# Optimization experiments

Hardware: AMD Instinct MI355X
Metric: run time of the kernel (lower is better)

## Reference

```python
import jax, jax.numpy as jnp
import numpy as np

B = 2048          # puzzles
E_PER = 1620      # 81 cells * 20 constraint neighbors
N = B * 81        # total nodes
NFEAT = 10


def _winit(key, fan_in, fan_out):
    s = (1.0 / np.sqrt(fan_in)).astype(np.float32) if isinstance(fan_in, np.ndarray) else 1.0 / np.sqrt(fan_in)
    return jax.random.uniform(key, (fan_in, fan_out), jnp.float32, -s, s)


def setup_inputs() -> dict:
    key = jax.random.key(0)
    ks = jax.random.split(key, 20)
    x = jax.random.normal(ks[0], (N, NFEAT), jnp.float32)
    # batched edge index [B, 2, E_PER]; values are global node ids
    edge_index = jax.random.randint(ks[1], (B, 2, E_PER), 0, N, dtype=jnp.int32)
    dims = [(NFEAT, 16), (16, 32), (32, 64), (64, 32), (32, 16)]
    params = {}
    for i, (ci, co) in enumerate(dims, start=1):
        params[f'W{i}'] = _winit(ks[2 * i], ci, co)
        params[f'b{i}'] = jnp.zeros((co,), jnp.float32)
    params['fW1'] = _winit(ks[14], 16, 16)
    params['fb1'] = jnp.zeros((16,), jnp.float32)
    params['fW2'] = _winit(ks[15], 16, 9)
    params['fb2'] = jnp.zeros((9,), jnp.float32)
    return {'x': x, 'edge_index': edge_index, **params}


def _gcn(h, W, b, src, dst, norm):
    # GCNConv: out[i] = sum_{j->i} norm_ij * (h_j W) + b   (self-loops included in src/dst)
    h = h @ W                                  # [N, Cout] small GEMM
    msg = h[src] * norm[:, None]               # gather + scale, [E+N, Cout]
    return jax.ops.segment_sum(msg, dst, num_segments=N) + b


def reference(x, edge_index, W1, b1, W2, b2, W3, b3, W4, b4, W5, b5, fW1, fb1, fW2, fb2):
    # replicate edge_index.permute(1,2,0).reshape(2,-1)
    ei = jnp.transpose(edge_index, (1, 2, 0)).reshape(2, -1)
    src, dst = ei[0], ei[1]
    # add self loops (PyG gcn_norm default)
    loop = jnp.arange(N, dtype=src.dtype)
    src = jnp.concatenate([src, loop])
    dst = jnp.concatenate([dst, loop])
    deg = jax.ops.segment_sum(jnp.ones(src.shape, x.dtype), dst, num_segments=N)
    dinv = jnp.where(deg > 0, jax.lax.rsqrt(jnp.maximum(deg, 1e-12)), 0.0)
    norm = dinv[src] * dinv[dst]               # shared across layers (same graph)
    h = jax.nn.relu(_gcn(x, W1, b1, src, dst, norm))
    h = jax.nn.relu(_gcn(h, W2, b2, src, dst, norm))
    h = jax.nn.relu(_gcn(h, W3, b3, src, dst, norm))
    h = jax.nn.relu(_gcn(h, W4, b4, src, dst, norm))
    h = jax.nn.relu(_gcn(h, W5, b5, src, dst, norm))
    h = h.reshape(-1, 16)
    h = jax.nn.relu(h @ fW1 + fb1)
    h = h @ fW2 + fb2
    return h.reshape(-1, 81, 9)
```

## Files before the change

### kernel.cpp

```cpp
#include <hip/hip_runtime.h>
#include <hip/hip_fp16.h>


#define NN    165888
#define NBAT  2048
#define EPER  1620
#define NEDGE (NBAT * EPER)
#define ETOT  (NEDGE + NN)
#define NBKT  648
#define NBLK  512
#define SCATE (4 * EPER)
#define SLICE 20736
#define BCAP  6144


__device__ inline void blk_scan256(int val, int& excl, int& total, int* sw) {
  int lane = threadIdx.x & 63, w = threadIdx.x >> 6;
  int x = val;
#pragma unroll
  for (int off = 1; off < 64; off <<= 1) {
    int y = __shfl_up(x, off);
    if (lane >= off) x += y;
  }
  if (lane == 63) sw[w] = x;
  __syncthreads();
  int woff = 0;
  if (w > 0) woff = sw[0];
  if (w > 1) woff += sw[1];
  if (w > 2) woff += sw[2];
  total = sw[0] + sw[1] + sw[2] + sw[3];
  excl = woff + x - val;
}

__device__ inline void pbase_scan(const int* __restrict__ btot, int* pb, int* sw) {
  int t = threadIdx.x;
  int e0 = 0, e1 = 0, e2 = 0, s = 0;
  if (t < 216) {
    e0 = btot[3 * t]; e1 = btot[3 * t + 1]; e2 = btot[3 * t + 2];
    s = e0 + e1 + e2;
  }
  int excl, tot;
  blk_scan256(s, excl, tot, sw);
  if (t < 216) {
    pb[3 * t]     = excl;
    pb[3 * t + 1] = excl + e0;
    pb[3 * t + 2] = excl + e0 + e1;
  }
  __syncthreads();
}


__global__ __launch_bounds__(256) void k_count(const int* __restrict__ ei,
                                               int* __restrict__ counts) {
  __shared__ int cnt[NBKT];
  int t = threadIdx.x;
  for (int k = t; k < NBKT; k += 256) cnt[k] = 0;
  __syncthreads();
  int b0 = blockIdx.x * 4;
  for (int b = b0; b < b0 + 4; ++b) {
    const int* dstp = ei + (size_t)b * (2 * EPER) + EPER;
    for (int e = t; e < EPER; e += 256) atomicAdd(&cnt[dstp[e] >> 8], 1);
  }
  __syncthreads();
  for (int k = t; k < NBKT; k += 256) counts[blockIdx.x * NBKT + k] = cnt[k];
}

__global__ __launch_bounds__(256) void k_scan(const int* __restrict__ counts,
                                              int* __restrict__ basesT,
                                              int* __restrict__ btot) {
  int bkt = blockIdx.x, t = threadIdx.x;
  int a = counts[(2 * t)     * NBKT + bkt];
  int b = counts[(2 * t + 1) * NBKT + bkt];
  __shared__ int sw[4];
  int excl, tot;
  blk_scan256(a + b, excl, tot, sw);
  basesT[bkt * NBLK + 2 * t]     = excl;
  basesT[bkt * NBLK + 2 * t + 1] = excl + a;
  if (t == 255) btot[bkt] = tot;
}

__global__ __launch_bounds__(256) void k_scat(const int* __restrict__ ei,
                                              const int* __restrict__ basesT,
                                              const int* __restrict__ btot,
                                              unsigned int* __restrict__ pairs) {
  __shared__ int pb[NBKT];
  __shared__ int sw[4];
  __shared__ int cnt[NBKT];
  __shared__ int lcur[NBKT];
  __shared__ int gdst[NBKT];
  __shared__ unsigned int sorted[SCATE];
  __shared__ unsigned short sbkt[SCATE];
  int t = threadIdx.x;
  for (int k = t; k < NBKT; k += 256) cnt[k] = 0;
  pbase_scan(btot, pb, sw);
  int b0 = blockIdx.x * 4;
  for (int b = b0; b < b0 + 4; ++b) {
    const int* dstp = ei + (size_t)b * (2 * EPER) + EPER;
    for (int e = t; e < EPER; e += 256) atomicAdd(&cnt[dstp[e] >> 8], 1);
  }
  __syncthreads();
  {
    int e0 = 0, e1 = 0, e2 = 0, s = 0;
    if (t < 216) {
      e0 = cnt[3 * t]; e1 = cnt[3 * t + 1]; e2 = cnt[3 * t + 2];
      s = e0 + e1 + e2;
    }
    int excl, tot;
    blk_scan256(s, excl, tot, sw);
    if (t < 216) {
      cnt[3 * t]     = excl;
      cnt[3 * t + 1] = excl + e0;
      cnt[3 * t + 2] = excl + e0 + e1;
    }
  }
  __syncthreads();
  for (int k = t; k < NBKT; k += 256) {
    int loc = cnt[k];
    gdst[k] = pb[k] + basesT[k * NBLK + blockIdx.x] - loc;
    lcur[k] = loc;
  }
  __syncthreads();
  for (int b = b0; b < b0 + 4; ++b) {
    const int* srcp = ei + (size_t)b * (2 * EPER);
    const int* dstp = srcp + EPER;
    for (int e = t; e < EPER; e += 256) {
      int d = dstp[e];
      int bk = d >> 8;
      int pos = atomicAdd(&lcur[bk], 1);
      sorted[pos] = (unsigned int)srcp[e] | ((unsigned int)(d & 255) << 24);
      sbkt[pos]   = (unsigned short)bk;
    }
  }
  __syncthreads();
  for (int k = t; k < SCATE; k += 256)
    pairs[gdst[sbkt[k]] + k] = sorted[k];
}

__global__ __launch_bounds__(256) void k_build(const unsigned int* __restrict__ pairs,
                                               const int* __restrict__ btot,
                                               const float* __restrict__ x,
                                               const float* __restrict__ W1,
                                               int* __restrict__ row_start,
                                               int* __restrict__ row_end,
                                               float* __restrict__ dinv,
                                               int* __restrict__ csr,
                                               __half* __restrict__ g0) {
  __shared__ int pb[NBKT];
  __shared__ int sw[4];
  __shared__ int cnt[256];
  __shared__ unsigned int sp[BCAP];
  __shared__ float sW[160];
  int bkt = blockIdx.x, t = threadIdx.x;
  cnt[t] = 0;
  if (t < 160) sW[t] = W1[t];
  pbase_scan(btot, pb, sw);
  int p0 = pb[bkt];
  int n  = btot[bkt];
  for (int k = t; k < n; k += 256) {
    unsigned int pr = pairs[p0 + k];
    if (k < BCAP) sp[k] = pr;
    atomicAdd(&cnt[pr >> 24], 1);
  }
  __syncthreads();
  int indeg = cnt[t];
  int excl, tot;
  blk_scan256(indeg, excl, tot, sw);
  int csrbase = p0 + bkt * 256;
  int rs   = csrbase + excl + t;
  int node = bkt * 256 + t;
  int d    = indeg + 1;
  float di = rsqrtf((float)d);
  row_start[node] = rs;
  row_end[node]   = rs + d;
  dinv[node] = di;
  csr[rs] = node;
  __syncthreads();
  cnt[t] = rs + 1;
  __syncthreads();
  for (int k = t; k < n; k += 256) {
    unsigned int pr = (k < BCAP) ? sp[k] : pairs[p0 + k];
    int pos = atomicAdd(&cnt[pr >> 24], 1);
    csr[pos] = (int)(pr & 0x00FFFFFFu);
  }
  float r[10];
#pragma unroll
  for (int k = 0; k < 10; ++k) r[k] = x[(size_t)node * 10 + k];
  float acc[16];
#pragma unroll
  for (int j = 0; j < 16; ++j) acc[j] = 0.0f;
#pragma unroll
  for (int k = 0; k < 10; ++k) {
    float rv = r[k];
#pragma unroll
    for (int j = 0; j < 16; ++j) acc[j] = fmaf(rv, sW[k * 16 + j], acc[j]);
  }
  __half* op = g0 + (size_t)node * 16;
  union { int4 v; __half2 h[4]; } pk;
#pragma unroll
  for (int half8 = 0; half8 < 2; ++half8) {
#pragma unroll
    for (int j = 0; j < 4; ++j)
      pk.h[j] = __floats2half2_rn(acc[half8 * 8 + 2 * j] * di,
                                  acc[half8 * 8 + 2 * j + 1] * di);
    *(int4*)(op + half8 * 8) = pk.v;
  }
}


template <int C, int EPI>
__device__ inline float4 agg_core_h(const __half* __restrict__ g,
                                    const int* __restrict__ csr,
                                    int rs, int re, int q, int gl) {
  constexpr int LG = C / 4;
  float4 acc = make_float4(0.f, 0.f, 0.f, 0.f);
  const __half* gq = g + (size_t)q * 4;
  int iters = 0;
  for (int p = rs; p < re; p += EPI) {
    ++iters;
    int m[EPI / LG];
#pragma unroll
    for (int u = 0; u < EPI / LG; ++u) {
      int idx = p + u * LG + q;
      m[u] = csr[idx < re ? idx : re - 1];
    }
    float2 v[EPI];
#pragma unroll
    for (int j = 0; j < EPI; ++j) {
      int s = __shfl(m[j / LG], gl + (j % LG));
      v[j] = *(const float2*)(gq + (size_t)s * C);
    }
#pragma unroll
    for (int j = 0; j < EPI; ++j) {
      const __half2* hp = (const __half2*)&v[j];
      float2 lo = __half22float2(hp[0]);
      float2 hi = __half22float2(hp[1]);
      acc.x += lo.x; acc.y += lo.y; acc.z += hi.x; acc.w += hi.y;
    }
  }
  float dups = (float)(iters * EPI - (re - rs));
  int slast = csr[re - 1];
  float2 vl = *(const float2*)(gq + (size_t)slast * C);
  const __half2* hp = (const __half2*)&vl;
  float2 lo = __half22float2(hp[0]);
  float2 hi = __half22float2(hp[1]);
  acc.x = fmaf(-dups, lo.x, acc.x);
  acc.y = fmaf(-dups, lo.y, acc.y);
  acc.z = fmaf(-dups, hi.x, acc.z);
  acc.w = fmaf(-dups, hi.y, acc.w);
  return acc;
}


__global__ __launch_bounds__(256) void k_agg_ep16(const __half* __restrict__ g,
                                                  const int* __restrict__ row_start,
                                                  const int* __restrict__ row_end,
                                                  const int* __restrict__ csr,
                                                  const float* __restrict__ dinv,
                                                  const float* __restrict__ bias,
                                                  __half* __restrict__ out) {
  constexpr int LG = 4, NPB = 64, SPB = SLICE / NPB;
  int t  = threadIdx.x;
  int q  = t & (LG - 1);
  int bi = blockIdx.x;
  int vb = (bi & 7) * SPB + (bi >> 3);
  int i  = vb * NPB + t / LG;
  int gl = (t & 63) & ~(LG - 1);
  float4 acc = agg_core_h<16, 16>(g, csr, row_start[i], row_end[i], q, gl);
  float di = dinv[i];
  float4 bb = *(const float4*)(bias + q * 4);
  acc.x = fmaxf(fmaf(di, acc.x, bb.x), 0.f) * di;
  acc.y = fmaxf(fmaf(di, acc.y, bb.y), 0.f) * di;
  acc.z = fmaxf(fmaf(di, acc.z, bb.z), 0.f) * di;
  acc.w = fmaxf(fmaf(di, acc.w, bb.w), 0.f) * di;
  union { int2 v; __half2 h[2]; } pk;
  pk.h[0] = __floats2half2_rn(acc.x, acc.y);
  pk.h[1] = __floats2half2_rn(acc.z, acc.w);
  *(int2*)(out + (size_t)i * 16 + q * 4) = pk.v;
}


__global__ __launch_bounds__(256) void k_agg_g2(const __half* __restrict__ g,
                                                const int* __restrict__ row_start,
                                                const int* __restrict__ row_end,
                                                const int* __restrict__ csr,
                                                const float* __restrict__ dinv,
                                                const float* __restrict__ W2,
                                                const float* __restrict__ b2,
                                                __half* __restrict__ out) {
  constexpr int CI = 16, CO = 32, LG = 4, NPB = 64, SPB = SLICE / NPB, RP = 20;
  __shared__ float sW[CI * CO];
  __shared__ float sB[CO];
  __shared__ float rows[NPB * RP];
  __shared__ float sdi[NPB];
  int t = threadIdx.x;
  for (int k = t; k < CI * CO; k += 256) sW[k] = W2[k];
  if (t < CO) sB[t] = b2[t];
  int bi = blockIdx.x;
  int vb = (bi & 7) * SPB + (bi >> 3);
  int nbase = vb * NPB;
  int q = t & (LG - 1), nl = t / LG;
  int i = nbase + nl;
  int gl = (t & 63) & ~(LG - 1);
  float4 acc = agg_core_h<16, 16>(g, csr, row_start[i], row_end[i], q, gl);
  float di = dinv[i];
  acc.x *= di; acc.y *= di; acc.z *= di; acc.w *= di;
  *(float4*)&rows[nl * RP + q * 4] = acc;
  if (q == 0) sdi[nl] = di;
  __syncthreads();
  int n2 = t >> 2, c = t & 3;
  float o[8];
#pragma unroll
  for (int j = 0; j < 8; ++j) o[j] = sB[c * 8 + j];
  const float* row = &rows[n2 * RP];
#pragma unroll
  for (int k = 0; k < CI; ++k) {
    float rv = row[k];
#pragma unroll
    for (int j = 0; j < 8; ++j) o[j] = fmaf(rv, sW[k * CO + c * 8 + j], o[j]);
  }
  float d2 = sdi[n2];
#pragma unroll
  for (int j = 0; j < 8; ++j) o[j] = fmaxf(o[j], 0.f) * d2;
  union { int4 v; __half2 h[4]; } pk;
#pragma unroll
  for (int j = 0; j < 4; ++j) pk.h[j] = __floats2half2_rn(o[2 * j], o[2 * j + 1]);
  *(int4*)(out + (size_t)(nbase + n2) * 32 + c * 8) = pk.v;
}


__global__ __launch_bounds__(256) void k_agg_g34(const __half* __restrict__ g,
                                                 const int* __restrict__ row_start,
                                                 const int* __restrict__ row_end,
                                                 const int* __restrict__ csr,
                                                 const float* __restrict__ dinv,
                                                 const float* __restrict__ W3,
                                                 const float* __restrict__ b3,
                                                 const float* __restrict__ W4,
                                                 __half* __restrict__ out) {
  constexpr int LG = 8, NPB = 32, SPB = SLICE / NPB, RP = 36, HP = 68;
  __shared__ float sW3[32 * 64];
  __shared__ float sW4[64 * 32];
  __shared__ float sB3[64];
  __shared__ float rows[NPB * RP];
  __shared__ float hrows[NPB * HP];
  __shared__ float sdi[NPB];
  int t = threadIdx.x;
  for (int k = t; k < 2048; k += 256) { sW3[k] = W3[k]; sW4[k] = W4[k]; }
  if (t < 64) sB3[t] = b3[t];
  int bi = blockIdx.x;
  int vb = (bi & 7) * SPB + (bi >> 3);
  int nbase = vb * NPB;
  int q = t & (LG - 1), nl = t / LG;
  int i = nbase + nl;
  int gl = (t & 63) & ~(LG - 1);
  float4 acc = agg_core_h<32, 16>(g, csr, row_start[i], row_end[i], q, gl);
  float di = dinv[i];
  acc.x *= di; acc.y *= di; acc.z *= di; acc.w *= di;
  *(float4*)&rows[nl * RP + q * 4] = acc;
  if (q == 0) sdi[nl] = di;
  __syncthreads();
  int n2 = t >> 3, c = t & 7;
  {
    float o[8];
#pragma unroll
    for (int j = 0; j < 8; ++j) o[j] = sB3[c * 8 + j];
    const float* row = &rows[n2 * RP];
#pragma unroll
    for (int k = 0; k < 32; ++k) {
      float rv = row[k];
#pragma unroll
      for (int j = 0; j < 8; ++j) o[j] = fmaf(rv, sW3[k * 64 + c * 8 + j], o[j]);
    }
    float* hp = &hrows[n2 * HP + c * 8];
#pragma unroll
    for (int j = 0; j < 8; ++j) hp[j] = fmaxf(o[j], 0.f);
  }
  __syncthreads();
  {
    float o[4] = {0.f, 0.f, 0.f, 0.f};
    const float* hp = &hrows[n2 * HP];
#pragma unroll
    for (int k = 0; k < 64; ++k) {
      float hv = hp[k];
#pragma unroll
      for (int j = 0; j < 4; ++j) o[j] = fmaf(hv, sW4[k * 32 + c * 4 + j], o[j]);
    }
    float d2 = sdi[n2];
#pragma unroll
    for (int j = 0; j < 4; ++j) o[j] *= d2;
    union { int2 v; __half2 h[2]; } pk;
    pk.h[0] = __floats2half2_rn(o[0], o[1]);
    pk.h[1] = __floats2half2_rn(o[2], o[3]);
    *(int2*)(out + (size_t)(nbase + n2) * 32 + c * 4) = pk.v;
  }
}


__global__ __launch_bounds__(256) void k_agg_g5(const __half* __restrict__ g,
                                                const int* __restrict__ row_start,
                                                const int* __restrict__ row_end,
                                                const int* __restrict__ csr,
                                                const float* __restrict__ dinv,
                                                const float* __restrict__ b4,
                                                const float* __restrict__ W5,
                                                __half* __restrict__ out) {
  constexpr int LG = 8, NPB = 32, SPB = SLICE / NPB, RP = 36;
  __shared__ float sW[32 * 16];
  __shared__ float rows[NPB * RP];
  __shared__ float sdi[NPB];
  int t = threadIdx.x;
  for (int k = t; k < 512; k += 256) sW[k] = W5[k];
  int bi = blockIdx.x;
  int vb = (bi & 7) * SPB + (bi >> 3);
  int nbase = vb * NPB;
  int q = t & (LG - 1), nl = t / LG;
  int i = nbase + nl;
  int gl = (t & 63) & ~(LG - 1);
  float4 acc = agg_core_h<32, 16>(g, csr, row_start[i], row_end[i], q, gl);
  float di = dinv[i];
  float4 bb = *(const float4*)(b4 + q * 4);
  acc.x = fmaxf(fmaf(di, acc.x, bb.x), 0.f);
  acc.y = fmaxf(fmaf(di, acc.y, bb.y), 0.f);
  acc.z = fmaxf(fmaf(di, acc.z, bb.z), 0.f);
  acc.w = fmaxf(fmaf(di, acc.w, bb.w), 0.f);
  *(float4*)&rows[nl * RP + q * 4] = acc;
  if (q == 0) sdi[nl] = di;
  __syncthreads();
  int n2 = t >> 3, c = t & 7;
  float o0 = 0.f, o1 = 0.f;
  const float* row = &rows[n2 * RP];
#pragma unroll
  for (int k = 0; k < 32; ++k) {
    float rv = row[k];
    o0 = fmaf(rv, sW[k * 16 + c * 2],     o0);
    o1 = fmaf(rv, sW[k * 16 + c * 2 + 1], o1);
  }
  float d2 = sdi[n2];
  *(__half2*)(out + (size_t)(nbase + n2) * 16 + c * 2)
      = __floats2half2_rn(o0 * d2, o1 * d2);
}


__global__ __launch_bounds__(256) void k_agg_mlp(const __half* __restrict__ g,
                                                 const int* __restrict__ row_start,
                                                 const int* __restrict__ row_end,
                                                 const int* __restrict__ csr,
                                                 const float* __restrict__ dinv,
                                                 const float* __restrict__ b5,
                                                 const float* __restrict__ fW1,
                                                 const float* __restrict__ fb1,
                                                 const float* __restrict__ fW2,
                                                 const float* __restrict__ fb2,
                                                 float* __restrict__ out) {
  constexpr int LG = 4, NPB = 64, SPB = SLICE / NPB, RP = 20;
  __shared__ float sW1[256], sW2[144], sB1[16], sB2[9];
  __shared__ float rows[NPB * RP];
  __shared__ float zrows[NPB * RP];
  __shared__ float ost[NPB * 9];
  int t = threadIdx.x;
  sW1[t] = fW1[t];
  if (t < 144) sW2[t] = fW2[t];
  if (t < 16)  sB1[t] = fb1[t];
  if (t < 9)   sB2[t] = fb2[t];
  int bi = blockIdx.x;
  int vb = (bi & 7) * SPB + (bi >> 3);
  int nbase = vb * NPB;
  int q = t & (LG - 1), nl = t / LG;
  int i = nbase + nl;
  int gl = (t & 63) & ~(LG - 1);
  float4 acc = agg_core_h<16, 16>(g, csr, row_start[i], row_end[i], q, gl);
  float di = dinv[i];
  float4 bb = *(const float4*)(b5 + q * 4);
  acc.x = fmaxf(fmaf(di, acc.x, bb.x), 0.f);
  acc.y = fmaxf(fmaf(di, acc.y, bb.y), 0.f);
  acc.z = fmaxf(fmaf(di, acc.z, bb.z), 0.f);
  acc.w = fmaxf(fmaf(di, acc.w, bb.w), 0.f);
  *(float4*)&rows[nl * RP + q * 4] = acc;
  __syncthreads();
  int n2 = t >> 2, c = t & 3;
  {
    float o[4];
#pragma unroll
    for (int j = 0; j < 4; ++j) o[j] = sB1[c * 4 + j];
    const float* row = &rows[n2 * RP];
#pragma unroll
    for (int k = 0; k < 16; ++k) {
      float rv = row[k];
#pragma unroll
      for (int j = 0; j < 4; ++j) o[j] = fmaf(rv, sW1[k * 16 + c * 4 + j], o[j]);
    }
    float* zp = &zrows[n2 * RP + c * 4];
#pragma unroll
    for (int j = 0; j < 4; ++j) zp[j] = fmaxf(o[j], 0.f);
  }
  __syncthreads();
  if (c < 3) {
    float o[3];
#pragma unroll
    for (int j = 0; j < 3; ++j) o[j] = sB2[c * 3 + j];
    const float* zp = &zrows[n2 * RP];
#pragma unroll
    for (int k = 0; k < 16; ++k) {
      float zv = zp[k];
#pragma unroll
      for (int j = 0; j < 3; ++j) o[j] = fmaf(zv, sW2[k * 9 + c * 3 + j], o[j]);
    }
#pragma unroll
    for (int j = 0; j < 3; ++j) ost[n2 * 9 + c * 3 + j] = o[j];
  }
  __syncthreads();
  float* ob = out + (size_t)nbase * 9;
  for (int k = t; k < NPB * 9; k += 256) ob[k] = ost[k];
}


extern "C" void kernel_launch(void* const* d_in, const int* in_sizes, int n_in,
                              void* d_out, int out_size, void* d_ws, size_t ws_size,
                              hipStream_t stream) {
  const float* x   = (const float*)d_in[0];
  const int*   ei  = (const int*)d_in[1];
  const float* W1  = (const float*)d_in[2];
  const float* b1  = (const float*)d_in[3];
  const float* W2  = (const float*)d_in[4];
  const float* b2  = (const float*)d_in[5];
  const float* W3  = (const float*)d_in[6];
  const float* b3  = (const float*)d_in[7];
  const float* W4  = (const float*)d_in[8];
  const float* b4  = (const float*)d_in[9];
  const float* W5  = (const float*)d_in[10];
  const float* b5  = (const float*)d_in[11];
  const float* fW1 = (const float*)d_in[12];
  const float* fb1 = (const float*)d_in[13];
  const float* fW2 = (const float*)d_in[14];
  const float* fb2 = (const float*)d_in[15];
  float* out = (float*)d_out;

  char* ws = (char*)d_ws;
  size_t off = 0;
  auto alloc = [&](size_t bytes) -> char* {
    char* p = ws + off;
    off += (bytes + 255) & ~(size_t)255;
    return p;
  };
  int*   counts  = (int*)  alloc((size_t)NBLK * NBKT * 4);
  int*   basesT  = (int*)  alloc((size_t)NBKT * NBLK * 4);
  int*   btot    = (int*)  alloc((size_t)NBKT * 4);
  unsigned int* pairs = (unsigned int*)alloc((size_t)NEDGE * 4);
  int*   rs_     = (int*)  alloc((size_t)NN * 4);
  int*   re_     = (int*)  alloc((size_t)NN * 4);
  float* dinv    = (float*)alloc((size_t)NN * 4);
  int*   csr     = (int*)  alloc((size_t)ETOT * 4);
  __half* H16a   = (__half*)alloc((size_t)NN * 16 * 2);
  __half* H16b   = (__half*)alloc((size_t)NN * 16 * 2);
  __half* H32a   = (__half*)alloc((size_t)NN * 32 * 2);
  __half* H32b   = (__half*)alloc((size_t)NN * 32 * 2);

  k_count<<<NBLK, 256, 0, stream>>>(ei, counts);
  k_scan <<<NBKT, 256, 0, stream>>>(counts, basesT, btot);
  k_scat <<<NBLK, 256, 0, stream>>>(ei, basesT, btot, pairs);
  k_build<<<NBKT, 256, 0, stream>>>(pairs, btot, x, W1, rs_, re_, dinv, csr, H16a);

  k_agg_ep16<<<NN / 64, 256, 0, stream>>>(H16a, rs_, re_, csr, dinv, b1, H16b);
  k_agg_g2<<<NN / 64, 256, 0, stream>>>(H16b, rs_, re_, csr, dinv, W2, b2, H32a);
  k_agg_g34<<<NN / 32, 256, 0, stream>>>(H32a, rs_, re_, csr, dinv, W3, b3, W4, H32b);
  k_agg_g5<<<NN / 32, 256, 0, stream>>>(H32b, rs_, re_, csr, dinv, b4, W5, H16a);
  k_agg_mlp<<<NN / 64, 256, 0, stream>>>(H16a, rs_, re_, csr, dinv, b5,
                                         fW1, fb1, fW2, fb2, out);
}
```

Measured before the change: 365.8 us.

## Widen per-lane gathers to 8 halfs and double nodes per block in aggregation kernels

The aggregation core now has each lane load 16 bytes (8 half channels) per neighbor instead of 8 bytes, so each node uses half as many lanes and each block covers twice as many nodes. Grid sizes are halved, edges per iteration drop from 16 to 8, and the fused dense epilogues are remapped so each thread computes twice as many outputs. The shared-memory row padding changes to odd strides (17/33/65) to avoid bank conflicts. The aim is fewer, wider memory transactions and less shuffle and index overhead per edge, at the cost of higher register pressure and less parallelism per node.

```diff
diff --git a/kernel.cpp b/kernel.cpp
--- a/kernel.cpp
+++ b/kernel.cpp
@@ -208,12 +208,14 @@
 
 
 template <int C, int EPI>
-__device__ inline float4 agg_core_h(const __half* __restrict__ g,
+__device__ inline void agg_core_h16(const __half* __restrict__ g,
                                     const int* __restrict__ csr,
-                                    int rs, int re, int q, int gl) {
-  constexpr int LG = C / 4;
-  float4 acc = make_float4(0.f, 0.f, 0.f, 0.f);
-  const __half* gq = g + (size_t)q * 4;
+                                    int rs, int re, int q, int gl,
+                                    float4& outLo, float4& outHi) {
+  constexpr int LG = C / 8;
+  float4 aLo = make_float4(0.f, 0.f, 0.f, 0.f);
+  float4 aHi = make_float4(0.f, 0.f, 0.f, 0.f);
+  const __half* gq = g + (size_t)q * 8;
   int iters = 0;
   for (int p = rs; p < re; p += EPI) {
     ++iters;
@@ -223,31 +225,36 @@
       int idx = p + u * LG + q;
       m[u] = csr[idx < re ? idx : re - 1];
     }
-    float2 v[EPI];
+    float4 v[EPI];
 #pragma unroll
     for (int j = 0; j < EPI; ++j) {
       int s = __shfl(m[j / LG], gl + (j % LG));
-      v[j] = *(const float2*)(gq + (size_t)s * C);
+      v[j] = *(const float4*)(gq + (size_t)s * C);
     }
 #pragma unroll
     for (int j = 0; j < EPI; ++j) {
       const __half2* hp = (const __half2*)&v[j];
-      float2 lo = __half22float2(hp[0]);
-      float2 hi = __half22float2(hp[1]);
-      acc.x += lo.x; acc.y += lo.y; acc.z += hi.x; acc.w += hi.y;
+      float2 f0 = __half22float2(hp[0]);
+      float2 f1 = __half22float2(hp[1]);
+      float2 f2 = __half22float2(hp[2]);
+      float2 f3 = __half22float2(hp[3]);
+      aLo.x += f0.x; aLo.y += f0.y; aLo.z += f1.x; aLo.w += f1.y;
+      aHi.x += f2.x; aHi.y += f2.y; aHi.z += f3.x; aHi.w += f3.y;
     }
   }
   float dups = (float)(iters * EPI - (re - rs));
   int slast = csr[re - 1];
-  float2 vl = *(const float2*)(gq + (size_t)slast * C);
+  float4 vl = *(const float4*)(gq + (size_t)slast * C);
   const __half2* hp = (const __half2*)&vl;
-  float2 lo = __half22float2(hp[0]);
-  float2 hi = __half22float2(hp[1]);
-  acc.x = fmaf(-dups, lo.x, acc.x);
-  acc.y = fmaf(-dups, lo.y, acc.y);
-  acc.z = fmaf(-dups, hi.x, acc.z);
-  acc.w = fmaf(-dups, hi.y, acc.w);
-  return acc;
+  float2 f0 = __half22float2(hp[0]);
+  float2 f1 = __half22float2(hp[1]);
+  float2 f2 = __half22float2(hp[2]);
+  float2 f3 = __half22float2(hp[3]);
+  aLo.x = fmaf(-dups, f0.x, aLo.x); aLo.y = fmaf(-dups, f0.y, aLo.y);
+  aLo.z = fmaf(-dups, f1.x, aLo.z); aLo.w = fmaf(-dups, f1.y, aLo.w);
+  aHi.x = fmaf(-dups, f2.x, aHi.x); aHi.y = fmaf(-dups, f2.y, aHi.y);
+  aHi.z = fmaf(-dups, f3.x, aHi.z); aHi.w = fmaf(-dups, f3.y, aHi.w);
+  outLo = aLo; outHi = aHi;
 }
 
 
@@ -258,24 +265,33 @@
                                                   const float* __restrict__ dinv,
                                                   const float* __restrict__ bias,
                                                   __half* __restrict__ out) {
-  constexpr int LG = 4, NPB = 64, SPB = SLICE / NPB;
+  constexpr int NPB = 128, SPB = SLICE / NPB;
   int t  = threadIdx.x;
-  int q  = t & (LG - 1);
+  int q  = t & 1;
   int bi = blockIdx.x;
   int vb = (bi & 7) * SPB + (bi >> 3);
-  int i  = vb * NPB + t / LG;
-  int gl = (t & 63) & ~(LG - 1);
-  float4 acc = agg_core_h<16, 16>(g, csr, row_start[i], row_end[i], q, gl);
+  int i  = vb * NPB + t / 2;
+  int gl = (t & 63) & ~1;
+  float4 aLo, aHi;
+  agg_core_h16<16, 8>(g, csr, row_start[i], row_end[i], q, gl, aLo, aHi);
   float di = dinv[i];
-  float4 bb = *(const float4*)(bias + q * 4);
-  acc.x = fmaxf(fmaf(di, acc.x, bb.x), 0.f) * di;
-  acc.y = fmaxf(fmaf(di, acc.y, bb.y), 0.f) * di;
-  acc.z = fmaxf(fmaf(di, acc.z, bb.z), 0.f) * di;
-  acc.w = fmaxf(fmaf(di, acc.w, bb.w), 0.f) * di;
-  union { int2 v; __half2 h[2]; } pk;
-  pk.h[0] = __floats2half2_rn(acc.x, acc.y);
-  pk.h[1] = __floats2half2_rn(acc.z, acc.w);
-  *(int2*)(out + (size_t)i * 16 + q * 4) = pk.v;
+  const float* bp = bias + q * 8;
+  float4 b0 = *(const float4*)bp;
+  float4 b1 = *(const float4*)(bp + 4);
+  aLo.x = fmaxf(fmaf(di, aLo.x, b0.x), 0.f) * di;
+  aLo.y = fmaxf(fmaf(di, aLo.y, b0.y), 0.f) * di;
+  aLo.z = fmaxf(fmaf(di, aLo.z, b0.z), 0.f) * di;
+  aLo.w = fmaxf(fmaf(di, aLo.w, b0.w), 0.f) * di;
+  aHi.x = fmaxf(fmaf(di, aHi.x, b1.x), 0.f) * di;
+  aHi.y = fmaxf(fmaf(di, aHi.y, b1.y), 0.f) * di;
+  aHi.z = fmaxf(fmaf(di, aHi.z, b1.z), 0.f) * di;
+  aHi.w = fmaxf(fmaf(di, aHi.w, b1.w), 0.f) * di;
+  union { int4 v; __half2 h[4]; } pk;
+  pk.h[0] = __floats2half2_rn(aLo.x, aLo.y);
+  pk.h[1] = __floats2half2_rn(aLo.z, aLo.w);
+  pk.h[2] = __floats2half2_rn(aHi.x, aHi.y);
+  pk.h[3] = __floats2half2_rn(aHi.z, aHi.w);
+  *(int4*)(out + (size_t)i * 16 + q * 8) = pk.v;
 }
 
 
@@ -287,7 +303,7 @@
                                                 const float* __restrict__ W2,
                                                 const float* __restrict__ b2,
                                                 __half* __restrict__ out) {
-  constexpr int CI = 16, CO = 32, LG = 4, NPB = 64, SPB = SLICE / NPB, RP = 20;
+  constexpr int CI = 16, CO = 32, NPB = 128, SPB = SLICE / NPB, RP = 17;
   __shared__ float sW[CI * CO];
   __shared__ float sB[CO];
   __shared__ float rows[NPB * RP];
@@ -298,33 +314,41 @@
   int bi = blockIdx.x;
   int vb = (bi & 7) * SPB + (bi >> 3);
   int nbase = vb * NPB;
-  int q = t & (LG - 1), nl = t / LG;
+  int q = t & 1, nl = t / 2;
   int i = nbase + nl;
-  int gl = (t & 63) & ~(LG - 1);
-  float4 acc = agg_core_h<16, 16>(g, csr, row_start[i], row_end[i], q, gl);
+  int gl = (t & 63) & ~1;
+  float4 aLo, aHi;
+  agg_core_h16<16, 8>(g, csr, row_start[i], row_end[i], q, gl, aLo, aHi);
   float di = dinv[i];
-  acc.x *= di; acc.y *= di; acc.z *= di; acc.w *= di;
-  *(float4*)&rows[nl * RP + q * 4] = acc;
+  aLo.x *= di; aLo.y *= di; aLo.z *= di; aLo.w *= di;
+  aHi.x *= di; aHi.y *= di; aHi.z *= di; aHi.w *= di;
+  *(float4*)&rows[nl * RP + q * 8]     = aLo;
+  *(float4*)&rows[nl * RP + q * 8 + 4] = aHi;
   if (q == 0) sdi[nl] = di;
   __syncthreads();
-  int n2 = t >> 2, c = t & 3;
-  float o[8];
-#pragma unroll
-  for (int j = 0; j < 8; ++j) o[j] = sB[c * 8 + j];
+  int n2 = t >> 1, c = t & 1;
+  float o[16];
+#pragma unroll
+  for (int j = 0; j < 16; ++j) o[j] = sB[c * 16 + j];
   const float* row = &rows[n2 * RP];
 #pragma unroll
   for (int k = 0; k < CI; ++k) {
     float rv = row[k];
 #pragma unroll
-    for (int j = 0; j < 8; ++j) o[j] = fmaf(rv, sW[k * CO + c * 8 + j], o[j]);
+    for (int j = 0; j < 16; ++j) o[j] = fmaf(rv, sW[k * CO + c * 16 + j], o[j]);
   }
   float d2 = sdi[n2];
 #pragma unroll
-  for (int j = 0; j < 8; ++j) o[j] = fmaxf(o[j], 0.f) * d2;
+  for (int j = 0; j < 16; ++j) o[j] = fmaxf(o[j], 0.f) * d2;
+  __half* op = out + (size_t)(nbase + n2) * 32 + c * 16;
   union { int4 v; __half2 h[4]; } pk;
 #pragma unroll
-  for (int j = 0; j < 4; ++j) pk.h[j] = __floats2half2_rn(o[2 * j], o[2 * j + 1]);
-  *(int4*)(out + (size_t)(nbase + n2) * 32 + c * 8) = pk.v;
+  for (int half8 = 0; half8 < 2; ++half8) {
+#pragma unroll
+    for (int j = 0; j < 4; ++j)
+      pk.h[j] = __floats2half2_rn(o[half8 * 8 + 2 * j], o[half8 * 8 + 2 * j + 1]);
+    *(int4*)(op + half8 * 8) = pk.v;
+  }
 }
 
 
@@ -337,7 +361,7 @@
                                                  const float* __restrict__ b3,
                                                  const float* __restrict__ W4,
                                                  __half* __restrict__ out) {
-  constexpr int LG = 8, NPB = 32, SPB = SLICE / NPB, RP = 36, HP = 68;
+  constexpr int NPB = 64, SPB = SLICE / NPB, RP = 33, HP = 65;
   __shared__ float sW3[32 * 64];
   __shared__ float sW4[64 * 32];
   __shared__ float sB3[64];
@@ -350,48 +374,50 @@
   int bi = blockIdx.x;
   int vb = (bi & 7) * SPB + (bi >> 3);
   int nbase = vb * NPB;
-  int q = t & (LG - 1), nl = t / LG;
+  int q = t & 3, nl = t / 4;
   int i = nbase + nl;
-  int gl = (t & 63) & ~(LG - 1);
-  float4 acc = agg_core_h<32, 16>(g, csr, row_start[i], row_end[i], q, gl);
+  int gl = (t & 63) & ~3;
+  float4 aLo, aHi;
+  agg_core_h16<32, 8>(g, csr, row_start[i], row_end[i], q, gl, aLo, aHi);
   float di = dinv[i];
-  acc.x *= di; acc.y *= di; acc.z *= di; acc.w *= di;
-  *(float4*)&rows[nl * RP + q * 4] = acc;
+  aLo.x *= di; aLo.y *= di; aLo.z *= di; aLo.w *= di;
+  aHi.x *= di; aHi.y *= di; aHi.z *= di; aHi.w *= di;
+  *(float4*)&rows[nl * RP + q * 8]     = aLo;
+  *(float4*)&rows[nl * RP + q * 8 + 4] = aHi;
   if (q == 0) sdi[nl] = di;
   __syncthreads();
-  int n2 = t >> 3, c = t & 7;
+  int n2 = t >> 2, c = t & 3;
   {
-    float o[8];
-#pragma unroll
-    for (int j = 0; j < 8; ++j) o[j] = sB3[c * 8 + j];
+    float o[16];
+#pragma unroll
+    for (int j = 0; j < 16; ++j) o[j] = sB3[c * 16 + j];
     const float* row = &rows[n2 * RP];
 #pragma unroll
     for (int k = 0; k < 32; ++k) {
       float rv = row[k];
 #pragma unroll
-      for (int j = 0; j < 8; ++j) o[j] = fmaf(rv, sW3[k * 64 + c * 8 + j], o[j]);
-    }
-    float* hp = &hrows[n2 * HP + c * 8];
-#pragma unroll
-    for (int j = 0; j < 8; ++j) hp[j] = fmaxf(o[j], 0.f);
+      for (int j = 0; j < 16; ++j) o[j] = fmaf(rv, sW3[k * 64 + c * 16 + j], o[j]);
+    }
+    float* hp = &hrows[n2 * HP + c * 16];
+#pragma unroll
+    for (int j = 0; j < 16; ++j) hp[j] = fmaxf(o[j], 0.f);
   }
   __syncthreads();
   {
-    float o[4] = {0.f, 0.f, 0.f, 0.f};
+    float o[8] = {0.f, 0.f, 0.f, 0.f, 0.f, 0.f, 0.f, 0.f};
     const float* hp = &hrows[n2 * HP];
 #pragma unroll
     for (int k = 0; k < 64; ++k) {
       float hv = hp[k];
 #pragma unroll
-      for (int j = 0; j < 4; ++j) o[j] = fmaf(hv, sW4[k * 32 + c * 4 + j], o[j]);
+      for (int j = 0; j < 8; ++j) o[j] = fmaf(hv, sW4[k * 32 + c * 8 + j], o[j]);
     }
     float d2 = sdi[n2];
-#pragma unroll
-    for (int j = 0; j < 4; ++j) o[j] *= d2;
-    union { int2 v; __half2 h[2]; } pk;
-    pk.h[0] = __floats2half2_rn(o[0], o[1]);
-    pk.h[1] = __floats2half2_rn(o[2], o[3]);
-    *(int2*)(out + (size_t)(nbase + n2) * 32 + c * 4) = pk.v;
+    union { int4 v; __half2 h[4]; } pk;
+#pragma unroll
+    for (int j = 0; j < 4; ++j)
+      pk.h[j] = __floats2half2_rn(o[2 * j] * d2, o[2 * j + 1] * d2);
+    *(int4*)(out + (size_t)(nbase + n2) * 32 + c * 8) = pk.v;
   }
 }
 
@@ -404,7 +430,7 @@
                                                 const float* __restrict__ b4,
                                                 const float* __restrict__ W5,
                                                 __half* __restrict__ out) {
-  constexpr int LG = 8, NPB = 32, SPB = SLICE / NPB, RP = 36;
+  constexpr int NPB = 64, SPB = SLICE / NPB, RP = 33;
   __shared__ float sW[32 * 16];
   __shared__ float rows[NPB * RP];
   __shared__ float sdi[NPB];
@@ -413,31 +439,41 @@
   int bi = blockIdx.x;
   int vb = (bi & 7) * SPB + (bi >> 3);
   int nbase = vb * NPB;
-  int q = t & (LG - 1), nl = t / LG;
+  int q = t & 3, nl = t / 4;
   int i = nbase + nl;
-  int gl = (t & 63) & ~(LG - 1);
-  float4 acc = agg_core_h<32, 16>(g, csr, row_start[i], row_end[i], q, gl);
+  int gl = (t & 63) & ~3;
+  float4 aLo, aHi;
+  agg_core_h16<32, 8>(g, csr, row_start[i], row_end[i], q, gl, aLo, aHi);
   float di = dinv[i];
-  float4 bb = *(const float4*)(b4 + q * 4);
-  acc.x = fmaxf(fmaf(di, acc.x, bb.x), 0.f);
-  acc.y = fmaxf(fmaf(di, acc.y, bb.y), 0.f);
-  acc.z = fmaxf(fmaf(di, acc.z, bb.z), 0.f);
-  acc.w = fmaxf(fmaf(di, acc.w, bb.w), 0.f);
-  *(float4*)&rows[nl * RP + q * 4] = acc;
+  const float* bp = b4 + q * 8;
+  float4 b0 = *(const float4*)bp;
+  float4 b1 = *(const float4*)(bp + 4);
+  aLo.x = fmaxf(fmaf(di, aLo.x, b0.x), 0.f);
+  aLo.y = fmaxf(fmaf(di, aLo.y, b0.y), 0.f);
+  aLo.z = fmaxf(fmaf(di, aLo.z, b0.z), 0.f);
+  aLo.w = fmaxf(fmaf(di, aLo.w, b0.w), 0.f);
+  aHi.x = fmaxf(fmaf(di, aHi.x, b1.x), 0.f);
+  aHi.y = fmaxf(fmaf(di, aHi.y, b1.y), 0.f);
+  aHi.z = fmaxf(fmaf(di, aHi.z, b1.z), 0.f);
+  aHi.w = fmaxf(fmaf(di, aHi.w, b1.w), 0.f);
+  *(float4*)&rows[nl * RP + q * 8]     = aLo;
+  *(float4*)&rows[nl * RP + q * 8 + 4] = aHi;
   if (q == 0) sdi[nl] = di;
   __syncthreads();
-  int n2 = t >> 3, c = t & 7;
-  float o0 = 0.f, o1 = 0.f;
+  int n2 = t >> 2, c = t & 3;
+  float o[4] = {0.f, 0.f, 0.f, 0.f};
   const float* row = &rows[n2 * RP];
 #pragma unroll
   for (int k = 0; k < 32; ++k) {
     float rv = row[k];
-    o0 = fmaf(rv, sW[k * 16 + c * 2],     o0);
-    o1 = fmaf(rv, sW[k * 16 + c * 2 + 1], o1);
+#pragma unroll
+    for (int j = 0; j < 4; ++j) o[j] = fmaf(rv, sW[k * 16 + c * 4 + j], o[j]);
   }
   float d2 = sdi[n2];
-  *(__half2*)(out + (size_t)(nbase + n2) * 16 + c * 2)
-      = __floats2half2_rn(o0 * d2, o1 * d2);
+  union { int2 v; __half2 h[2]; } pk;
+  pk.h[0] = __floats2half2_rn(o[0] * d2, o[1] * d2);
+  pk.h[1] = __floats2half2_rn(o[2] * d2, o[3] * d2);
+  *(int2*)(out + (size_t)(nbase + n2) * 16 + c * 4) = pk.v;
 }
 
 
@@ -452,7 +488,7 @@
                                                  const float* __restrict__ fW2,
                                                  const float* __restrict__ fb2,
                                                  float* __restrict__ out) {
-  constexpr int LG = 4, NPB = 64, SPB = SLICE / NPB, RP = 20;
+  constexpr int NPB = 128, SPB = SLICE / NPB, RP = 17;
   __shared__ float sW1[256], sW2[144], sB1[16], sB2[9];
   __shared__ float rows[NPB * RP];
   __shared__ float zrows[NPB * RP];
@@ -465,48 +501,70 @@
   int bi = blockIdx.x;
   int vb = (bi & 7) * SPB + (bi >> 3);
   int nbase = vb * NPB;
-  int q = t & (LG - 1), nl = t / LG;
+  int q = t & 1, nl = t / 2;
   int i = nbase + nl;
-  int gl = (t & 63) & ~(LG - 1);
-  float4 acc = agg_core_h<16, 16>(g, csr, row_start[i], row_end[i], q, gl);
+  int gl = (t & 63) & ~1;
+  float4 aLo, aHi;
+  agg_core_h16<16, 8>(g, csr, row_start[i], row_end[i], q, gl, aLo, aHi);
   float di = dinv[i];
-  float4 bb = *(const float4*)(b5 + q * 4);
-  acc.x = fmaxf(fmaf(di, acc.x, bb.x), 0.f);
-  acc.y = fmaxf(fmaf(di, acc.y, bb.y), 0.f);
-  acc.z = fmaxf(fmaf(di, acc.z, bb.z), 0.f);
-  acc.w = fmaxf(fmaf(di, acc.w, bb.w), 0.f);
-  *(float4*)&rows[nl * RP + q * 4] = acc;
-  __syncthreads();
-  int n2 = t >> 2, c = t & 3;
+  const float* bp = b5 + q * 8;
+  float4 b0 = *(const float4*)bp;
+  float4 b1 = *(const float4*)(bp + 4);
+  aLo.x = fmaxf(fmaf(di, aLo.x, b0.x), 0.f);
+  aLo.y = fmaxf(fmaf(di, aLo.y, b0.y), 0.f);
+  aLo.z = fmaxf(fmaf(di, aLo.z, b0.z), 0.f);
+  aLo.w = fmaxf(fmaf(di, aLo.w, b0.w), 0.f);
+  aHi.x = fmaxf(fmaf(di, aHi.x, b1.x), 0.f);
+  aHi.y = fmaxf(fmaf(di, aHi.y, b1.y), 0.f);
+  aHi.z = fmaxf(fmaf(di, aHi.z, b1.z), 0.f);
+  aHi.w = fmaxf(fmaf(di, aHi.w, b1.w), 0.f);
+  *(float4*)&rows[nl * RP + q * 8]     = aLo;
+  *(float4*)&rows[nl * RP + q * 8 + 4] = aHi;
+  __syncthreads();
+  int n2 = t >> 1, c = t & 1;
   {
-    float o[4];
-#pragma unroll
-    for (int j = 0; j < 4; ++j) o[j] = sB1[c * 4 + j];
+    float o[8];
+#pragma unroll
+    for (int j = 0; j < 8; ++j) o[j] = sB1[c * 8 + j];
     const float* row = &rows[n2 * RP];
 #pragma unroll
     for (int k = 0; k < 16; ++k) {
       float rv = row[k];
 #pragma unroll
-      for (int j = 0; j < 4; ++j) o[j] = fmaf(rv, sW1[k * 16 + c * 4 + j], o[j]);
-    }
-    float* zp = &zrows[n2 * RP + c * 4];
-#pragma unroll
-    for (int j = 0; j < 4; ++j) zp[j] = fmaxf(o[j], 0.f);
-  }
-  __syncthreads();
-  if (c < 3) {
-    float o[3];
-#pragma unroll
-    for (int j = 0; j < 3; ++j) o[j] = sB2[c * 3 + j];
+      for (int j = 0; j < 8; ++j) o[j] = fmaf(rv, sW1[k * 16 + c * 8 + j], o[j]);
+    }
+    float* zp = &zrows[n2 * RP + c * 8];
+#pragma unroll
+    for (int j = 0; j < 8; ++j) zp[j] = fmaxf(o[j], 0.f);
+  }
+  __syncthreads();
+  {
     const float* zp = &zrows[n2 * RP];
-#pragma unroll
-    for (int k = 0; k < 16; ++k) {
-      float zv = zp[k];
-#pragma unroll
-      for (int j = 0; j < 3; ++j) o[j] = fmaf(zv, sW2[k * 9 + c * 3 + j], o[j]);
-    }
-#pragma unroll
-    for (int j = 0; j < 3; ++j) ost[n2 * 9 + c * 3 + j] = o[j];
+    if (c == 0) {
+      float o[5];
+#pragma unroll
+      for (int j = 0; j < 5; ++j) o[j] = sB2[j];
+#pragma unroll
+      for (int k = 0; k < 16; ++k) {
+        float zv = zp[k];
+#pragma unroll
+        for (int j = 0; j < 5; ++j) o[j] = fmaf(zv, sW2[k * 9 + j], o[j]);
+      }
+#pragma unroll
+      for (int j = 0; j < 5; ++j) ost[n2 * 9 + j] = o[j];
+    } else {
+      float o[4];
+#pragma unroll
+      for (int j = 0; j < 4; ++j) o[j] = sB2[5 + j];
+#pragma unroll
+      for (int k = 0; k < 16; ++k) {
+        float zv = zp[k];
+#pragma unroll
+        for (int j = 0; j < 4; ++j) o[j] = fmaf(zv, sW2[k * 9 + 5 + j], o[j]);
+      }
+#pragma unroll
+      for (int j = 0; j < 4; ++j) ost[n2 * 9 + 5 + j] = o[j];
+    }
   }
   __syncthreads();
   float* ob = out + (size_t)nbase * 9;
@@ -560,10 +618,10 @@
   k_scat <<<NBLK, 256, 0, stream>>>(ei, basesT, btot, pairs);
   k_build<<<NBKT, 256, 0, stream>>>(pairs, btot, x, W1, rs_, re_, dinv, csr, H16a);
 
-  k_agg_ep16<<<NN / 64, 256, 0, stream>>>(H16a, rs_, re_, csr, dinv, b1, H16b);
-  k_agg_g2<<<NN / 64, 256, 0, stream>>>(H16b, rs_, re_, csr, dinv, W2, b2, H32a);
-  k_agg_g34<<<NN / 32, 256, 0, stream>>>(H32a, rs_, re_, csr, dinv, W3, b3, W4, H32b);
-  k_agg_g5<<<NN / 32, 256, 0, stream>>>(H32b, rs_, re_, csr, dinv, b4, W5, H16a);
-  k_agg_mlp<<<NN / 64, 256, 0, stream>>>(H16a, rs_, re_, csr, dinv, b5,
-                                         fW1, fb1, fW2, fb2, out);
-}
+  k_agg_ep16<<<NN / 128, 256, 0, stream>>>(H16a, rs_, re_, csr, dinv, b1, H16b);
+  k_agg_g2<<<NN / 128, 256, 0, stream>>>(H16b, rs_, re_, csr, dinv, W2, b2, H32a);
+  k_agg_g34<<<NN / 64, 256, 0, stream>>>(H32a, rs_, re_, csr, dinv, W3, b3, W4, H32b);
+  k_agg_g5<<<NN / 64, 256, 0, stream>>>(H32b, rs_, re_, csr, dinv, b4, W5, H16a);
+  k_agg_mlp<<<NN / 128, 256, 0, stream>>>(H16a, rs_, re_, csr, dinv, b5,
+                                          fW1, fb1, fW2, fb2, out);
+}
```

After: 413.3 us. +13.0%, slower.
